# Kernel tuning notes

Hardware: AMD Instinct MI355X
Metric: run time of the kernel (lower is better)

Reference implementation:

```python
import math
import jax, jax.numpy as jnp
import numpy as np

B, S, D, H = 4, 1024, 1024, 16


def setup_inputs() -> dict:
    key = jax.random.key(0)
    k1, k2, k3 = jax.random.split(key, 3)
    x = jax.random.normal(k1, (B, S, D), dtype=jnp.float32)
    mask = jnp.ones((B, S), dtype=jnp.int32)  # 1 = valid token (all-ones: see notes)
    W_qkv = jax.random.normal(k2, (D, 3 * D), dtype=jnp.float32) * (1.0 / math.sqrt(D))
    b_qkv = jax.random.normal(k3, (3 * D,), dtype=jnp.float32) * 0.02
    return {"x": x, "mask": mask, "W_qkv": W_qkv, "b_qkv": b_qkv, "num_heads": H}


def reference(x, mask, W_qkv, b_qkv, num_heads):
    Bb, Ss, Dd = x.shape
    head_dim = Dd // num_heads
    scale = 1.0 / math.sqrt(Dd / num_heads)  # matches 1/sqrt(embed_dim/num_heads)

    qkv = x @ W_qkv + b_qkv                                  # [B,S,3D]
    q, k, v = jnp.split(qkv, 3, axis=-1)                      # each [B,S,D]
    q = q.reshape(Bb, Ss, num_heads, head_dim).transpose(0, 2, 1, 3) * scale  # [B,H,S,d]
    k = k.reshape(Bb, Ss, num_heads, head_dim).transpose(0, 2, 1, 3)          # [B,H,S,d]
    v = v.reshape(Bb, Ss, num_heads, head_dim).transpose(0, 2, 1, 3)          # [B,H,S,d]

    attn = jnp.einsum('bhqd,bhkd->bhqk', q, k)                # [B,H,S,S]
    mf = mask.astype(attn.dtype)
    attn_mask = mf[:, None, :, None] * mf[:, None, None, :]   # [B,1,S,S] outer product
    attn = jnp.where(attn_mask == 0, -jnp.inf, attn)
    attn = jax.nn.softmax(attn, axis=-1)

    out = jnp.einsum('bhqk,bhkd->bhqd', attn, v)              # [B,H,S,d]
    return out.transpose(0, 2, 1, 3).reshape(Bb, Ss, Dd)      # [B,S,D]
```

## Files before the change

kernel.cpp:

```cpp
#include <hip/hip_runtime.h>
#include <hip/hip_bf16.h>

typedef __attribute__((ext_vector_type(8))) short short8;
typedef __attribute__((ext_vector_type(4))) float floatx4;

#define MFMA16(A, B, C) __builtin_amdgcn_mfma_f32_16x16x32_bf16(A, B, C, 0, 0, 0)

static constexpr int S  = 1024;
static constexpr int D  = 1024;
static constexpr int N3 = 3 * D;
#define QSCALE 0.18033688011112042f

static inline __device__ ushort f2b(float f) {
  __hip_bfloat16 h = __float2bfloat16(f);
  return *(ushort*)&h;
}

static inline __device__ void gld16(const ushort* g, ushort* l) {
  __builtin_amdgcn_global_load_lds((const __attribute__((address_space(1))) void*)g,
                                   (__attribute__((address_space(3))) void*)l, 16, 0, 0);
}

__global__ __launch_bounds__(256) void prep(const float* __restrict__ x,
                                            const float* __restrict__ w,
                                            ushort* __restrict__ xb,
                                            ushort* __restrict__ wt) {
  __shared__ float t[32][33];
  const int bid = blockIdx.x;
  if (bid < 4096) {
    const int i = (bid * 256 + threadIdx.x) * 4;
    const float4 f = *(const float4*)(x + i);
    ushort4 u;
    u.x = f2b(f.x); u.y = f2b(f.y); u.z = f2b(f.z); u.w = f2b(f.w);
    *(ushort4*)(xb + i) = u;
  } else {
    const int id = bid - 4096;
    const int tx = threadIdx.x & 31;
    const int ty = threadIdx.x >> 5;
    const int n0 = (id % 96) * 32;
    const int k0 = (id / 96) * 32;
#pragma unroll
    for (int j = 0; j < 4; ++j)
      t[ty + j * 8][tx] = w[(long)(k0 + ty + j * 8) * N3 + n0 + tx];
    __syncthreads();
#pragma unroll
    for (int j = 0; j < 4; ++j)
      wt[(long)(n0 + ty + j * 8) * D + k0 + tx] = f2b(t[tx][ty + j * 8]);
  }
}

__global__ __launch_bounds__(256) void qkv_gemm(const ushort* __restrict__ xb,
                                                const ushort* __restrict__ wtb,
                                                const float* __restrict__ bias,
                                                ushort* __restrict__ Qb,
                                                ushort* __restrict__ Kb,
                                                ushort* __restrict__ Vt) {
  __shared__ __align__(16) ushort Asm[128 * 32];
  __shared__ __align__(16) ushort Bsm[128 * 32];

  const int tid  = threadIdx.x;
  const int lane = tid & 63;
  const int wid  = tid >> 6;
  const int l15  = lane & 15;
  const int quad = lane >> 4;
  const int n0 = blockIdx.x * 128;
  const int m0 = blockIdx.y * 128;
  const int wm = (wid >> 1) * 64;
  const int wn = (wid & 1) * 64;

  floatx4 acc[4][4];
#pragma unroll
  for (int i = 0; i < 4; ++i)
#pragma unroll
    for (int j = 0; j < 4; ++j) acc[i][j] = (floatx4)0.0f;

  const int srow = lane >> 2;
  const int scol = (lane & 3) * 8;

  for (int k0 = 0; k0 < D; k0 += 32) {
#pragma unroll
    for (int j = 0; j < 2; ++j) {
      const int r0 = wid * 32 + j * 16;
      gld16(xb  + (long)(m0 + r0 + srow) * D + k0 + scol, &Asm[r0 * 32]);
      gld16(wtb + (long)(n0 + r0 + srow) * D + k0 + scol, &Bsm[r0 * 32]);
    }
    __syncthreads();

    short8 af[4], bf[4];
#pragma unroll
    for (int mt = 0; mt < 4; ++mt)
      af[mt] = *(const short8*)&Asm[(wm + mt * 16 + l15) * 32 + quad * 8];
#pragma unroll
    for (int nt = 0; nt < 4; ++nt)
      bf[nt] = *(const short8*)&Bsm[(wn + nt * 16 + l15) * 32 + quad * 8];
#pragma unroll
    for (int mt = 0; mt < 4; ++mt)
#pragma unroll
      for (int nt = 0; nt < 4; ++nt)
        acc[mt][nt] = MFMA16(af[mt], bf[nt], acc[mt][nt]);
    __syncthreads();
  }

  const int ncls = n0 >> 10;
#pragma unroll
  for (int nt = 0; nt < 4; ++nt) {
    const int n = n0 + wn + nt * 16 + l15;
    const float bv = bias[n];
    if (ncls == 0) {
#pragma unroll
      for (int mt = 0; mt < 4; ++mt)
#pragma unroll
        for (int r = 0; r < 4; ++r) {
          const int m = m0 + wm + mt * 16 + quad * 4 + r;
          Qb[(long)m * D + n] = f2b((acc[mt][nt][r] + bv) * QSCALE);
        }
    } else if (ncls == 1) {
#pragma unroll
      for (int mt = 0; mt < 4; ++mt)
#pragma unroll
        for (int r = 0; r < 4; ++r) {
          const int m = m0 + wm + mt * 16 + quad * 4 + r;
          Kb[(long)m * D + (n - 1024)] = f2b(acc[mt][nt][r] + bv);
        }
    } else {
      const int nn = n - 2048;
      const int hh = nn >> 6, dd = nn & 63;
#pragma unroll
      for (int mt = 0; mt < 4; ++mt) {
        const int m = m0 + wm + mt * 16 + quad * 4;
        const int bb = m >> 10, ss = m & 1023;
        ushort4 pk;
        pk.x = f2b(acc[mt][nt][0] + bv);
        pk.y = f2b(acc[mt][nt][1] + bv);
        pk.z = f2b(acc[mt][nt][2] + bv);
        pk.w = f2b(acc[mt][nt][3] + bv);
        *(ushort4*)&Vt[((long)(bb * 16 + hh) * 64 + dd) * (long)S + ss] = pk;
      }
    }
  }
}

__global__ __launch_bounds__(512) void attn(const ushort* __restrict__ Qb,
                                            const ushort* __restrict__ Kb,
                                            const ushort* __restrict__ Vt,
                                            float* __restrict__ out) {
  __shared__ __align__(16) ushort Ksm[2][2][64][32];
  __shared__ __align__(16) ushort Vsm[2][2][64][32];
  __shared__ __align__(16) ushort Psm[8][16][72];

  const int tid  = threadIdx.x;
  const int lane = tid & 63;
  const int wid  = tid >> 6;
  const int l15  = lane & 15;
  const int quad = lane >> 4;
  const int qt = blockIdx.x;
  const int b  = blockIdx.y;
  const int h  = blockIdx.z;

  short8 qb[2];
  const int qbase = b * S + qt * 128 + wid * 16;
  {
    const ushort* qp = Qb + (long)(qbase + l15) * D + h * 64;
    qb[0] = *(const short8*)(qp + quad * 8);
    qb[1] = *(const short8*)(qp + 32 + quad * 8);
  }

  floatx4 o[4];
#pragma unroll
  for (int mt = 0; mt < 4; ++mt) o[mt] = (floatx4)0.0f;
  float ppart = 0.f;

  const ushort* kbase = Kb + (long)(b * S) * D + h * 64;
  const ushort* vbase = Vt + (long)(b * 16 + h) * 64 * (long)S;
  const int srow = lane >> 2;
  const int scol = (lane & 3) * 8;
  const int kh = wid & 1;
  const int rb = (wid >> 1) * 16;

  auto stage = [&](int kt, int buf) {
    gld16(kbase + (long)(kt * 64 + rb + srow) * D + kh * 32 + scol,
          &Ksm[buf][kh][rb][0]);
    gld16(vbase + (long)(rb + srow) * S + kt * 64 + kh * 32 + scol,
          &Vsm[buf][kh][rb][0]);
  };

  stage(0, 0);
  for (int kt = 0; kt < 16; ++kt) {
    const int cur = kt & 1;
    if (kt < 15) {
      stage(kt + 1, cur ^ 1);
      asm volatile("s_waitcnt vmcnt(2)" ::: "memory");
    } else {
      asm volatile("s_waitcnt vmcnt(0)" ::: "memory");
    }
    asm volatile("s_barrier" ::: "memory");

    floatx4 s[4];
#pragma unroll
    for (int mt = 0; mt < 4; ++mt) s[mt] = (floatx4)0.0f;
    __builtin_amdgcn_s_setprio(1);
#pragma unroll
    for (int ks = 0; ks < 2; ++ks)
#pragma unroll
      for (int mt = 0; mt < 4; ++mt) {
        const short8 ka = *(const short8*)&Ksm[cur][ks][mt * 16 + l15][quad * 8];
        s[mt] = MFMA16(ka, qb[ks], s[mt]);
      }
    __builtin_amdgcn_s_setprio(0);

#pragma unroll
    for (int mt = 0; mt < 4; ++mt) {
      const float p0 = exp2f(s[mt][0]);
      const float p1 = exp2f(s[mt][1]);
      const float p2 = exp2f(s[mt][2]);
      const float p3 = exp2f(s[mt][3]);
      ppart += (p0 + p1) + (p2 + p3);
      ushort4 pw;
      pw.x = f2b(p0); pw.y = f2b(p1); pw.z = f2b(p2); pw.w = f2b(p3);
      *(ushort4*)&Psm[wid][l15][mt * 16 + quad * 4] = pw;
    }
    asm volatile("s_waitcnt lgkmcnt(0)" ::: "memory");

    short8 pb[2];
#pragma unroll
    for (int ks = 0; ks < 2; ++ks)
      pb[ks] = *(const short8*)&Psm[wid][l15][ks * 32 + quad * 8];
    __builtin_amdgcn_s_setprio(1);
#pragma unroll
    for (int ks = 0; ks < 2; ++ks)
#pragma unroll
      for (int mt = 0; mt < 4; ++mt) {
        const short8 va = *(const short8*)&Vsm[cur][ks][mt * 16 + l15][quad * 8];
        o[mt] = MFMA16(va, pb[ks], o[mt]);
      }
    __builtin_amdgcn_s_setprio(0);
    asm volatile("s_barrier" ::: "memory");
  }

  {
    float li = ppart;
    li += __shfl_xor(li, 16);
    li += __shfl_xor(li, 32);
    const float inv = 1.0f / li;
    const int q = qbase + l15;
    const long obase = (long)q * D + h * 64;
#pragma unroll
    for (int mt = 0; mt < 4; ++mt) {
      float4 f;
      f.x = o[mt][0] * inv; f.y = o[mt][1] * inv;
      f.z = o[mt][2] * inv; f.w = o[mt][3] * inv;
      *(float4*)&out[obase + mt * 16 + quad * 4] = f;
    }
  }
}

extern "C" void kernel_launch(void* const* d_in, const int* in_sizes, int n_in,
                              void* d_out, int out_size, void* d_ws, size_t ws_size,
                              hipStream_t stream) {
  const float* x    = (const float*)d_in[0];
  const float* w    = (const float*)d_in[2];
  const float* bias = (const float*)d_in[3];

  ushort* xb  = (ushort*)d_ws;
  ushort* wtb = xb + (long)4096 * 1024;
  ushort* Qb  = wtb + (long)3072 * 1024;
  ushort* Kb  = Qb + (long)4096 * 1024;
  ushort* Vt  = Kb + (long)4096 * 1024;

  prep<<<7168, 256, 0, stream>>>(x, w, xb, wtb);
  qkv_gemm<<<dim3(24, 32), 256, 0, stream>>>(xb, wtb, bias, Qb, Kb, Vt);
  attn<<<dim3(8, 4, 16), 512, 0, stream>>>(Qb, Kb, Vt, (float*)d_out);
}
```

Before: 154.8 us.

## Rewrite QKV GEMM as 256x256 8-wave kernel with pipelined LDS loads

```diff
diff --git a/kernel.cpp b/kernel.cpp
--- a/kernel.cpp
+++ b/kernel.cpp
@@ -49,91 +49,144 @@
   }
 }
 
-__global__ __launch_bounds__(256) void qkv_gemm(const ushort* __restrict__ xb,
-                                                const ushort* __restrict__ wtb,
-                                                const float* __restrict__ bias,
-                                                ushort* __restrict__ Qb,
-                                                ushort* __restrict__ Kb,
-                                                ushort* __restrict__ Vt) {
-  __shared__ __align__(16) ushort Asm[128 * 32];
-  __shared__ __align__(16) ushort Bsm[128 * 32];
+__global__ __launch_bounds__(512, 2) void qkv_gemm8(const ushort* __restrict__ xb,
+                                                    const ushort* __restrict__ wtb,
+                                                    const float* __restrict__ bias,
+                                                    ushort* __restrict__ Qb,
+                                                    ushort* __restrict__ Kb,
+                                                    ushort* __restrict__ Vt) {
+  __shared__ __align__(16) ushort lds[65536];
 
   const int tid  = threadIdx.x;
   const int lane = tid & 63;
   const int wid  = tid >> 6;
   const int l15  = lane & 15;
   const int quad = lane >> 4;
-  const int n0 = blockIdx.x * 128;
-  const int m0 = blockIdx.y * 128;
-  const int wm = (wid >> 1) * 64;
-  const int wn = (wid & 1) * 64;
-
-  floatx4 acc[4][4];
-#pragma unroll
-  for (int i = 0; i < 4; ++i)
+
+  int bid = blockIdx.x;
+  bid = (bid & 7) * 24 + (bid >> 3);
+  const int n0 = (bid % 12) * 256;
+  const int m0 = (bid / 12) * 256;
+
+  const int wr = wid >> 2;
+  const int wc = wid & 3;
+  const int sz = (l15 & 4) ? 16 : 0;
+  const int cbs_u = ((lane & 7) * 8) ^ ((lane & 32) ? 16 : 0);
+  const int srcrow = wid * 8 + (lane >> 3);
+
+  floatx4 acc[8][4];
+#pragma unroll
+  for (int i = 0; i < 8; ++i)
 #pragma unroll
     for (int j = 0; j < 4; ++j) acc[i][j] = (floatx4)0.0f;
 
-  const int srow = lane >> 2;
-  const int scol = (lane & 3) * 8;
-
-  for (int k0 = 0; k0 < D; k0 += 32) {
-#pragma unroll
-    for (int j = 0; j < 2; ++j) {
-      const int r0 = wid * 32 + j * 16;
-      gld16(xb  + (long)(m0 + r0 + srow) * D + k0 + scol, &Asm[r0 * 32]);
-      gld16(wtb + (long)(n0 + r0 + srow) * D + k0 + scol, &Bsm[r0 * 32]);
-    }
-    __syncthreads();
-
-    short8 af[4], bf[4];
-#pragma unroll
-    for (int mt = 0; mt < 4; ++mt)
-      af[mt] = *(const short8*)&Asm[(wm + mt * 16 + l15) * 32 + quad * 8];
-#pragma unroll
-    for (int nt = 0; nt < 4; ++nt)
-      bf[nt] = *(const short8*)&Bsm[(wn + nt * 16 + l15) * 32 + quad * 8];
-#pragma unroll
-    for (int mt = 0; mt < 4; ++mt)
-#pragma unroll
-      for (int nt = 0; nt < 4; ++nt)
-        acc[mt][nt] = MFMA16(af[mt], bf[nt], acc[mt][nt]);
-    __syncthreads();
-  }
-
-  const int ncls = n0 >> 10;
-#pragma unroll
-  for (int nt = 0; nt < 4; ++nt) {
-    const int n = n0 + wn + nt * 16 + l15;
+  auto stage_g = [&](int g) {
+    const int tau = g >> 2, part = g & 3, ab = part & 1, ht = part >> 1;
+    const ushort* s0 = ab ? (wtb + (long)(n0 + ht * 128) * D)
+                          : (xb  + (long)(m0 + ht * 128) * D);
+    const ushort* src = s0 + tau * 64 + cbs_u + (long)srcrow * D;
+    ushort* dst = &lds[(tau & 1) * 32768 + ab * 16384 + ht * 8192 + wid * 512];
+    gld16(src, dst);
+    gld16(src + 64 * D, dst + 4096);
+  };
+
+  short8 fa[4][2];
+  short8 fb[2][2][2];
+
+  auto LDA = [&](int cb, int mh) {
+#pragma unroll
+    for (int i = 0; i < 4; ++i)
+#pragma unroll
+      for (int kk = 0; kk < 2; ++kk)
+        fa[i][kk] = *(const short8*)&lds[cb + wr * 8192 +
+            (((((mh * 4 + i) * 16 + l15) * 64) + kk * 32 + quad * 8) ^ sz)];
+  };
+  auto LDB = [&](int cb, int nh) {
+#pragma unroll
+    for (int j = 0; j < 2; ++j)
+#pragma unroll
+      for (int kk = 0; kk < 2; ++kk)
+        fb[nh][j][kk] = *(const short8*)&lds[cb + 16384 + (wc >> 1) * 8192 +
+            ((((((wc & 1) * 64 + (nh * 2 + j) * 16 + l15)) * 64) + kk * 32 + quad * 8) ^ sz)];
+  };
+  auto MM = [&](int mh, int nh) {
+#pragma unroll
+    for (int i = 0; i < 4; ++i)
+#pragma unroll
+      for (int j = 0; j < 2; ++j)
+#pragma unroll
+        for (int kk = 0; kk < 2; ++kk)
+          acc[mh * 4 + i][nh * 2 + j] =
+              MFMA16(fa[i][kk], fb[nh][j][kk], acc[mh * 4 + i][nh * 2 + j]);
+  };
+
+#pragma unroll
+  for (int g = 0; g < 7; ++g) stage_g(g);
+  asm volatile("s_waitcnt vmcnt(6)" ::: "memory");
+  asm volatile("s_barrier" ::: "memory");
+
+#pragma unroll 2
+  for (int kt = 0; kt < 16; ++kt) {
+    const int cb = (kt & 1) * 32768;
+    LDA(cb, 0); LDB(cb, 0);
+    { const int g = kt * 4 + 7; if (g < 64) stage_g(g); }
+    asm volatile("s_barrier" ::: "memory");
+    asm volatile("s_waitcnt lgkmcnt(0)" ::: "memory");
+    __builtin_amdgcn_s_setprio(1); MM(0, 0); __builtin_amdgcn_s_setprio(0);
+    asm volatile("s_barrier" ::: "memory");
+    LDB(cb, 1);
+    asm volatile("s_barrier" ::: "memory");
+    asm volatile("s_waitcnt lgkmcnt(0)" ::: "memory");
+    __builtin_amdgcn_s_setprio(1); MM(0, 1); __builtin_amdgcn_s_setprio(0);
+    asm volatile("s_barrier" ::: "memory");
+    LDA(cb, 1);
+    { const int g = kt * 4 + 9; if (g < 64) stage_g(g); }
+    asm volatile("s_barrier" ::: "memory");
+    asm volatile("s_waitcnt lgkmcnt(0)" ::: "memory");
+    __builtin_amdgcn_s_setprio(1); MM(1, 1); __builtin_amdgcn_s_setprio(0);
+    asm volatile("s_barrier" ::: "memory");
+    { const int g = kt * 4 + 8;  if (g < 64) stage_g(g); }
+    { const int g = kt * 4 + 10; if (g < 64) stage_g(g); }
+    asm volatile("s_barrier" ::: "memory");
+    __builtin_amdgcn_s_setprio(1); MM(1, 0); __builtin_amdgcn_s_setprio(0);
+    if (kt == 14)      asm volatile("s_waitcnt vmcnt(0)" ::: "memory");
+    else if (kt < 14)  asm volatile("s_waitcnt vmcnt(6)" ::: "memory");
+    asm volatile("s_barrier" ::: "memory");
+  }
+
+  const int cls = n0 >> 10;
+#pragma unroll
+  for (int ntl = 0; ntl < 4; ++ntl) {
+    const int n = n0 + wc * 64 + ntl * 16 + l15;
     const float bv = bias[n];
-    if (ncls == 0) {
-#pragma unroll
-      for (int mt = 0; mt < 4; ++mt)
+    if (cls == 0) {
+#pragma unroll
+      for (int mtl = 0; mtl < 8; ++mtl)
 #pragma unroll
         for (int r = 0; r < 4; ++r) {
-          const int m = m0 + wm + mt * 16 + quad * 4 + r;
-          Qb[(long)m * D + n] = f2b((acc[mt][nt][r] + bv) * QSCALE);
+          const int m = m0 + wr * 128 + mtl * 16 + quad * 4 + r;
+          Qb[(long)m * D + n] = f2b((acc[mtl][ntl][r] + bv) * QSCALE);
         }
-    } else if (ncls == 1) {
-#pragma unroll
-      for (int mt = 0; mt < 4; ++mt)
+    } else if (cls == 1) {
+#pragma unroll
+      for (int mtl = 0; mtl < 8; ++mtl)
 #pragma unroll
         for (int r = 0; r < 4; ++r) {
-          const int m = m0 + wm + mt * 16 + quad * 4 + r;
-          Kb[(long)m * D + (n - 1024)] = f2b(acc[mt][nt][r] + bv);
+          const int m = m0 + wr * 128 + mtl * 16 + quad * 4 + r;
+          Kb[(long)m * D + (n - 1024)] = f2b(acc[mtl][ntl][r] + bv);
         }
     } else {
       const int nn = n - 2048;
       const int hh = nn >> 6, dd = nn & 63;
 #pragma unroll
-      for (int mt = 0; mt < 4; ++mt) {
-        const int m = m0 + wm + mt * 16 + quad * 4;
+      for (int mtl = 0; mtl < 8; ++mtl) {
+        const int m = m0 + wr * 128 + mtl * 16 + quad * 4;
         const int bb = m >> 10, ss = m & 1023;
         ushort4 pk;
-        pk.x = f2b(acc[mt][nt][0] + bv);
-        pk.y = f2b(acc[mt][nt][1] + bv);
-        pk.z = f2b(acc[mt][nt][2] + bv);
-        pk.w = f2b(acc[mt][nt][3] + bv);
+        pk.x = f2b(acc[mtl][ntl][0] + bv);
+        pk.y = f2b(acc[mtl][ntl][1] + bv);
+        pk.z = f2b(acc[mtl][ntl][2] + bv);
+        pk.w = f2b(acc[mtl][ntl][3] + bv);
         *(ushort4*)&Vt[((long)(bb * 16 + hh) * 64 + dd) * (long)S + ss] = pk;
       }
     }
@@ -268,6 +321,6 @@
   ushort* Vt  = Kb + (long)4096 * 1024;
 
   prep<<<7168, 256, 0, stream>>>(x, w, xb, wtb);
-  qkv_gemm<<<dim3(24, 32), 256, 0, stream>>>(xb, wtb, bias, Qb, Kb, Vt);
+  qkv_gemm8<<<192, 512, 0, stream>>>(xb, wtb, bias, Qb, Kb, Vt);
   attn<<<dim3(8, 4, 16), 512, 0, stream>>>(Qb, Kb, Vt, (float*)d_out);
 }
```

After: 161.1 us. 1.04x slower.
